# Kernel optimization log

Hardware: AMD Instinct MI355X
Metric: run time of the kernel (lower is better)

The kernel has to match this reference:

```python
import jax, jax.numpy as jnp
import numpy as np

N = 100000     # total points
PBS = 500      # point_batch_size (hard-coded in module)
K = 100        # num_neighbors
KP = 15        # num_kernel_points
EPS = 1e-5


def _bn(x, g, b, axes):
    # torch BatchNorm in training mode: batch stats, biased variance
    m = jnp.mean(x, axis=axes, keepdims=True)
    v = jnp.var(x, axis=axes, keepdims=True)
    return (x - m) / jnp.sqrt(v + EPS) * g + b


def setup_inputs() -> dict:
    key = jax.random.key(0)
    ks = jax.random.split(key, 16)
    rn = lambda k, sh, s=1.0: jax.random.normal(k, sh, jnp.float32) * s
    return {
        "pts": rn(ks[0], (N, 3)),
        "normal": rn(ks[1], (N, 3)),
        "kp_points": rn(ks[2], (KP, 3)),
        "kp_weights": rn(ks[3], (KP, 3, 128), 0.3),
        "kp_sigma": jnp.float32(1.0),
        "conv1_w": rn(ks[4], (1024, 128), 128 ** -0.5),
        "conv1_b": rn(ks[5], (1024,), 0.02),
        "bn1_g": jnp.ones((1024,), jnp.float32),
        "bn1_b": jnp.zeros((1024,), jnp.float32),
        "fc1_w": rn(ks[6], (512, 1024), 1024 ** -0.5),
        "fc1_b": rn(ks[7], (512,), 0.02),
        "bn4_g": jnp.ones((512,), jnp.float32),
        "bn4_b": jnp.zeros((512,), jnp.float32),
        "fc2_w": rn(ks[8], (256, 512), 512 ** -0.5),
        "fc2_b": rn(ks[9], (256,), 0.02),
        "bn5_g": jnp.ones((256,), jnp.float32),
        "bn5_b": jnp.zeros((256,), jnp.float32),
        "fc3_w": rn(ks[10], (3, 256), 256 ** -0.5),
        "fc3_b": rn(ks[11], (3,), 0.02),
        "index": jax.random.randint(ks[12], (PBS,), 0, N, jnp.int32),
    }


def reference(pts, normal, kp_points, kp_weights, kp_sigma,
              conv1_w, conv1_b, bn1_g, bn1_b,
              fc1_w, fc1_b, bn4_g, bn4_b,
              fc2_w, fc2_b, bn5_g, bn5_b,
              fc3_w, fc3_b, index):
    sel = pts[index]                                               # [B,3]
    # L-inf pairwise distance and kNN (topk of -dist, as in the torch code)
    dist = jnp.max(jnp.abs(sel[:, None, :] - pts[None, :, :]), axis=-1)  # [B,N]
    _, nbr = jax.lax.top_k(-dist, K)                               # [B,K]
    rel = pts[nbr] - sel[:, None, :]                               # [B,K,3]

    # KPConv: gaussian weights vs kernel points, per-kernel-point linear map
    d2 = jnp.sum((rel[:, :, None, :] - kp_points[None, None]) ** 2, axis=-1)  # [B,K,KP]
    w = jnp.exp(-0.5 * d2 / (kp_sigma ** 2))
    wf = rel[:, :, None, :] * w[..., None]                         # [B,K,KP,3]
    h = jax.nn.relu(jnp.einsum('bnkc,kco->bno', wf, kp_weights))   # [B,K,128]

    # 1x1 conv 128->1024, relu then BN over (batch, points) per channel
    h = jnp.einsum('bnc,oc->bno', h, conv1_w) + conv1_b            # [B,K,1024]
    h = _bn(jax.nn.relu(h), bn1_g, bn1_b, (0, 1))
    feat = jnp.max(h, axis=1)                                      # [B,1024]

    feat = _bn(jax.nn.relu(feat @ fc1_w.T + fc1_b), bn4_g, bn4_b, (0,))
    feat = _bn(jax.nn.relu(feat @ fc2_w.T + fc2_b), bn5_g, bn5_b, (0,))
    feat = feat @ fc3_w.T + fc3_b                                  # [B,3]
    return feat, normal[index]
```

## Files before the change

kernel.cpp:

```cpp
#include <hip/hip_runtime.h>
#include <hip/hip_fp16.h>

#define NPTS 100000
#define NB 500
#define KNN 100
#define KPN 15
#define C1 128
#define C2 1024
#define C3 512
#define C4 256

#define G 64
#define NCELLS (G * G * G)
#define GB 5.0f
#define GINVH ((float)G / (2.f * GB))
#define CAND_CAP 2048

typedef _Float16 half8 __attribute__((ext_vector_type(8)));
typedef float f32x4 __attribute__((ext_vector_type(4)));

__device__ __forceinline__ int cell_coord(float x) {
  int c = (int)floorf((x + GB) * GINVH);
  return min(max(c, 0), G - 1);
}
__device__ __forceinline__ int cell_of(float x, float y, float z) {
  return (cell_coord(x) << 12) | (cell_coord(y) << 6) | cell_coord(z);
}

__global__ __launch_bounds__(256) void prep_kernel(
    const float* __restrict__ pts, const float* __restrict__ normal,
    const int* __restrict__ index, const float* __restrict__ w1,
    const float* __restrict__ kpw, float* __restrict__ sel,
    float* __restrict__ out2, __half* __restrict__ wh,
    __half* __restrict__ kpwT_hi, __half* __restrict__ kpwT_lo,
    unsigned* __restrict__ cnt) {
  int i = blockIdx.x * 256 + threadIdx.x;
  if (i < NB) {
    int ix = index[i];
    sel[i * 3 + 0] = pts[3 * ix + 0];
    sel[i * 3 + 1] = pts[3 * ix + 1];
    sel[i * 3 + 2] = pts[3 * ix + 2];
    out2[i * 3 + 0] = normal[3 * ix + 0];
    out2[i * 3 + 1] = normal[3 * ix + 1];
    out2[i * 3 + 2] = normal[3 * ix + 2];
  }
  if (i < C2 * C1) wh[i] = __float2half(w1[i]);
  if (i < 128 * 64) {
    int o = i >> 6, j = i & 63;
    float v = (j < 45) ? kpw[j * 128 + o] : 0.f;
    __half hi = __float2half_rn(v);
    kpwT_hi[i] = hi;
    kpwT_lo[i] = __float2half_rn(v - __half2float(hi));
  }
  if (i < NPTS)
    atomicAdd(&cnt[cell_of(pts[3 * i], pts[3 * i + 1], pts[3 * i + 2])], 1u);
}

__global__ __launch_bounds__(256) void grid_scan1_kernel(
    const unsigned* __restrict__ cnt, unsigned* __restrict__ cursor,
    unsigned* __restrict__ chunktot) {
  const int tid = threadIdx.x;
  int base = blockIdx.x * 1024 + tid * 4;
  unsigned c0 = cnt[base], c1 = cnt[base + 1], c2 = cnt[base + 2],
           c3 = cnt[base + 3];
  unsigned tot = c0 + c1 + c2 + c3;
  __shared__ unsigned sb[256];
  sb[tid] = tot;
  __syncthreads();
  for (int off = 1; off < 256; off <<= 1) {
    unsigned add = (tid >= off) ? sb[tid - off] : 0u;
    __syncthreads();
    sb[tid] += add;
    __syncthreads();
  }
  unsigned excl = sb[tid] - tot;
  cursor[base] = excl;
  cursor[base + 1] = excl + c0;
  cursor[base + 2] = excl + c0 + c1;
  cursor[base + 3] = excl + c0 + c1 + c2;
  if (tid == 255) chunktot[blockIdx.x] = sb[255];
}

__global__ __launch_bounds__(256) void grid_scan2_kernel(
    const unsigned* __restrict__ chunktot, unsigned* __restrict__ chunkoff) {
  const int tid = threadIdx.x;
  unsigned v = chunktot[tid];
  __shared__ unsigned sb[256];
  sb[tid] = v;
  __syncthreads();
  for (int off = 1; off < 256; off <<= 1) {
    unsigned add = (tid >= off) ? sb[tid - off] : 0u;
    __syncthreads();
    sb[tid] += add;
    __syncthreads();
  }
  chunkoff[tid] = sb[tid] - v;
}

__global__ __launch_bounds__(256) void grid_scan3_kernel(
    unsigned* __restrict__ cursor, const unsigned* __restrict__ chunkoff) {
  unsigned off = chunkoff[blockIdx.x];
  int base = blockIdx.x * 1024 + threadIdx.x * 4;
#pragma unroll
  for (int j = 0; j < 4; ++j) cursor[base + j] += off;
}

__global__ __launch_bounds__(256) void grid_scatter_kernel(
    const float* __restrict__ pts, unsigned* __restrict__ cursor,
    float4* __restrict__ sorted) {
  int i = blockIdx.x * 256 + threadIdx.x;
  if (i >= NPTS) return;
  float x = pts[3 * i], y = pts[3 * i + 1], z = pts[3 * i + 2];
  unsigned pos = atomicAdd(&cursor[cell_of(x, y, z)], 1u);
  sorted[pos] = make_float4(x, y, z, __int_as_float(i));
}

__device__ __forceinline__ unsigned linf_bits(float px, float py, float pz,
                                              float sx, float sy, float sz) {
  float dx = fabsf(px - sx), dy = fabsf(py - sy), dz = fabsf(pz - sz);
  return __float_as_uint(fmaxf(fmaxf(dx, dy), dz));
}

__global__ __launch_bounds__(256) void knn_kernel(
    const float4* __restrict__ sorted, const unsigned* __restrict__ cnt,
    const unsigned* __restrict__ cursor,
    const float* __restrict__ sel, int* __restrict__ nbr) {
  const int b = blockIdx.x;
  const int tid = threadIdx.x;
  __shared__ unsigned cbits[CAND_CAP];
  __shared__ int cidx[CAND_CAP];
  __shared__ unsigned hist[4096];
  __shared__ unsigned scanbuf[256];
  __shared__ int s_total, s_m, s_mc, s_chunk;
  __shared__ unsigned s_excl, s_bub;

  const float qx = sel[b * 3 + 0], qy = sel[b * 3 + 1], qz = sel[b * 3 + 2];
  const int qcx = cell_coord(qx), qcy = cell_coord(qy), qcz = cell_coord(qz);

  if (tid == 0) s_total = 0;
  __syncthreads();
  int s = 1;
  int pxlo = 1, pxhi = 0, pylo = 1, pyhi = 0, pzlo = 1, pzhi = 0;
  int xlo, xhi, ylo, yhi, zlo, zhi;
  for (;;) {
    xlo = max(qcx - s, 0); xhi = min(qcx + s, G - 1);
    ylo = max(qcy - s, 0); yhi = min(qcy + s, G - 1);
    zlo = max(qcz - s, 0); zhi = min(qcz + s, G - 1);
    int nx = xhi - xlo + 1, ny = yhi - ylo + 1, nz = zhi - zlo + 1;
    int ncell = nx * ny * nz;
    unsigned local = 0;
    for (int ci = tid; ci < ncell; ci += 256) {
      int cz = ci % nz;
      int r = ci / nz;
      int cy = r % ny;
      int cx = r / ny;
      int ax = xlo + cx, ay = ylo + cy, az = zlo + cz;
      if (ax >= pxlo && ax <= pxhi && ay >= pylo && ay <= pyhi &&
          az >= pzlo && az <= pzhi)
        continue;
      local += cnt[(ax << 12) | (ay << 6) | az];
    }
#pragma unroll
    for (int off = 32; off; off >>= 1) local += __shfl_down(local, off);
    if ((tid & 63) == 0) atomicAdd(&s_total, (int)local);
    __syncthreads();
    if (s_total >= KNN || (xlo == 0 && ylo == 0 && zlo == 0 && xhi == G - 1 &&
                           yhi == G - 1 && zhi == G - 1))
      break;
    pxlo = xlo; pxhi = xhi; pylo = ylo; pyhi = yhi; pzlo = zlo; pzhi = zhi;
    ++s;
    __syncthreads();
  }

  if (tid == 0) s_m = 0;
  __syncthreads();
  {
    int nx = xhi - xlo + 1, ny = yhi - ylo + 1, nz = zhi - zlo + 1;
    int ncell = nx * ny * nz;
    for (int ci = tid; ci < ncell; ci += 256) {
      int cz = ci % nz;
      int r = ci / nz;
      int cy = r % ny;
      int cx = r / ny;
      int cell = ((xlo + cx) << 12) | ((ylo + cy) << 6) | (zlo + cz);
      unsigned end = cursor[cell];
      unsigned beg = end - cnt[cell];
      int k = (int)(end - beg);
      if (k > 0) {
        int e0 = atomicAdd(&s_m, k);
        for (unsigned p = beg; p < end; ++p, ++e0) {
          if (e0 < CAND_CAP) {
            float4 f = sorted[p];
            cbits[e0] = linf_bits(f.x, f.y, f.z, qx, qy, qz);
            cidx[e0] = __float_as_int(f.w);
          }
        }
      }
    }
  }
  __syncthreads();
  int m = s_m < CAND_CAP ? s_m : CAND_CAP;

  for (int j = tid; j < 4096; j += 256) hist[j] = 0;
  __syncthreads();
  for (int e = tid; e < m; e += 256) atomicAdd(&hist[cbits[e] >> 19], 1u);
  __syncthreads();
  unsigned csum = 0;
  {
    int c0 = tid * 16;
#pragma unroll
    for (int j = 0; j < 16; ++j) csum += hist[c0 + j];
  }
  scanbuf[tid] = csum;
  __syncthreads();
  for (int off = 1; off < 256; off <<= 1) {
    unsigned add = (tid >= off) ? scanbuf[tid - off] : 0u;
    __syncthreads();
    scanbuf[tid] += add;
    __syncthreads();
  }
  {
    unsigned incl = scanbuf[tid], excl = incl - csum;
    if (excl < KNN && KNN <= incl) {
      s_chunk = tid;
      s_excl = excl;
    }
  }
  __syncthreads();
  if (tid == 0) {
    unsigned cum = s_excl;
    int bin = s_chunk * 16;
    while (cum + hist[bin] < KNN) {
      cum += hist[bin];
      ++bin;
    }
    s_bub = (unsigned)(bin + 1) << 19;
  }
  __syncthreads();

  const unsigned bub = s_bub;
  const float dub = __uint_as_float(bub);
  if (tid == 0) s_mc = 0;
  __syncthreads();
  {
    int xlo2 = min(max((int)floorf((qx - dub + GB) * GINVH), 0), G - 1);
    int xhi2 = min(max((int)floorf((qx + dub + GB) * GINVH), 0), G - 1);
    int ylo2 = min(max((int)floorf((qy - dub + GB) * GINVH), 0), G - 1);
    int yhi2 = min(max((int)floorf((qy + dub + GB) * GINVH), 0), G - 1);
    int zlo2 = min(max((int)floorf((qz - dub + GB) * GINVH), 0), G - 1);
    int zhi2 = min(max((int)floorf((qz + dub + GB) * GINVH), 0), G - 1);
    int nx = xhi2 - xlo2 + 1, ny = yhi2 - ylo2 + 1, nz = zhi2 - zlo2 + 1;
    int ncell = nx * ny * nz;
    for (int ci = tid; ci < ncell; ci += 256) {
      int cz = ci % nz;
      int r = ci / nz;
      int cy = r % ny;
      int cx = r / ny;
      int cell = ((xlo2 + cx) << 12) | ((ylo2 + cy) << 6) | (zlo2 + cz);
      unsigned end = cursor[cell];
      unsigned beg = end - cnt[cell];
      for (unsigned p = beg; p < end; ++p) {
        float4 f = sorted[p];
        unsigned bits = linf_bits(f.x, f.y, f.z, qx, qy, qz);
        if (bits < bub) {
          int e = atomicAdd(&s_mc, 1);
          if (e < CAND_CAP) {
            cbits[e] = bits;
            cidx[e] = __float_as_int(f.w);
          }
        }
      }
    }
  }
  __syncthreads();
  int mc = s_mc < CAND_CAP ? s_mc : CAND_CAP;

  for (int c = tid; c < mc; c += 256) {
    unsigned bc = cbits[c];
    int ic = cidx[c];
    int rank = 0;
    for (int j = 0; j < mc; ++j) {
      unsigned bj = cbits[j];
      rank += (bj < bc || (bj == bc && cidx[j] < ic)) ? 1 : 0;
    }
    if (rank < KNN) nbr[b * KNN + rank] = ic;
  }
}

__global__ __launch_bounds__(512) void kpconv_conv1_kernel(
    const float* __restrict__ pts, const float* __restrict__ sel,
    const int* __restrict__ nbr, const float* __restrict__ kp_points,
    const __half* __restrict__ kpwT_hi, const __half* __restrict__ kpwT_lo,
    const float* __restrict__ kp_sigma, const __half* __restrict__ wh,
    const float* __restrict__ bias, float* __restrict__ featmax,
    float* __restrict__ featmin, float* __restrict__ bnsum,
    float* __restrict__ bnsq) {
  const int b = blockIdx.x;
  const int tid = threadIdx.x;
  const int wave = tid >> 6, lane = tid & 63;
  const int lr = lane & 15, quad = lane >> 4;

  __shared__ __align__(16) char smem[71168];
  __half* As_hi = (__half*)smem;
  __half* As_lo = As_hi + 112 * 72;
  __half* Bs_hi = As_lo + 112 * 72;
  __half* Bs_lo = Bs_hi + 128 * 72;
  float* rel = (float*)(Bs_lo + 128 * 72);
  float* kpp = rel + 100 * 4;
  __half* Hs = (__half*)smem;
  __half* Ws = Hs + 112 * 136;

  for (int i = tid; i < 128 * 8; i += 512) {
    int row = i >> 3, seg = i & 7;
    *(float4*)&Bs_hi[row * 72 + seg * 8] =
        *(const float4*)&kpwT_hi[row * 64 + seg * 8];
    *(float4*)&Bs_lo[row * 72 + seg * 8] =
        *(const float4*)&kpwT_lo[row * 64 + seg * 8];
  }
  {
    float4 z = make_float4(0.f, 0.f, 0.f, 0.f);
    for (int i = tid; i < 112 * 8; i += 512) {
      int row = i >> 3, seg = i & 7;
      *(float4*)&As_hi[row * 72 + seg * 8] = z;
      *(float4*)&As_lo[row * 72 + seg * 8] = z;
    }
  }
  if (tid < 45) kpp[tid] = kp_points[tid];
  if (tid < 100) {
    int idx = nbr[b * KNN + tid];
    rel[tid * 4 + 0] = pts[3 * idx + 0] - sel[b * 3 + 0];
    rel[tid * 4 + 1] = pts[3 * idx + 1] - sel[b * 3 + 1];
    rel[tid * 4 + 2] = pts[3 * idx + 2] - sel[b * 3 + 2];
  }
  __syncthreads();

  const float sg = kp_sigma[0];
  const float inv2s2 = -0.5f / (sg * sg);
  for (int i = tid; i < 100 * KPN; i += 512) {
    int k = i / KPN, p = i - k * KPN;
    float rx = rel[k * 4 + 0] - kpp[p * 3 + 0];
    float ry = rel[k * 4 + 1] - kpp[p * 3 + 1];
    float rz = rel[k * 4 + 2] - kpp[p * 3 + 2];
    float w = expf(inv2s2 * (rx * rx + ry * ry + rz * rz));
#pragma unroll
    for (int c = 0; c < 3; ++c) {
      float a = rel[k * 4 + c] * w;
      __half hi = __float2half_rn(a);
      As_hi[k * 72 + p * 3 + c] = hi;
      As_lo[k * 72 + p * 3 + c] = __float2half_rn(a - __half2float(hi));
    }
  }
  __syncthreads();

  f32x4 acc1[7];
#pragma unroll
  for (int m = 0; m < 7; ++m) acc1[m] = (f32x4)(0.f);
#pragma unroll
  for (int s = 0; s < 2; ++s) {
    int boff = (wave * 16 + lr) * 72 + s * 32 + quad * 8;
    half8 bhi = *(const half8*)&Bs_hi[boff];
    half8 blo = *(const half8*)&Bs_lo[boff];
#pragma unroll
    for (int m = 0; m < 7; ++m) {
      int aoff = (m * 16 + lr) * 72 + s * 32 + quad * 8;
      half8 ahi = *(const half8*)&As_hi[aoff];
      half8 alo = *(const half8*)&As_lo[aoff];
      acc1[m] = __builtin_amdgcn_mfma_f32_16x16x32_f16(ahi, bhi, acc1[m], 0, 0, 0);
      acc1[m] = __builtin_amdgcn_mfma_f32_16x16x32_f16(ahi, blo, acc1[m], 0, 0, 0);
      acc1[m] = __builtin_amdgcn_mfma_f32_16x16x32_f16(alo, bhi, acc1[m], 0, 0, 0);
    }
  }
  __syncthreads();

  {
    int col = wave * 16 + lr;
#pragma unroll
    for (int m = 0; m < 7; ++m)
#pragma unroll
      for (int r = 0; r < 4; ++r) {
        int row = m * 16 + quad * 4 + r;
        Hs[row * 136 + col] = __float2half_rn(fmaxf(acc1[m][r], 0.f));
      }
  }

  for (int c = 0; c < 8; ++c) {
    __syncthreads();
    for (int i = tid; i < 128 * 16; i += 512) {
      int row = i >> 4, seg = i & 15;
      *(float4*)&Ws[row * 136 + seg * 8] =
          *(const float4*)&wh[(c * 128 + row) * 128 + seg * 8];
    }
    __syncthreads();

    f32x4 acc2[7];
#pragma unroll
    for (int m = 0; m < 7; ++m) acc2[m] = (f32x4)(0.f);
#pragma unroll
    for (int s = 0; s < 4; ++s) {
      half8 bfrag =
          *(const half8*)&Ws[(wave * 16 + lr) * 136 + s * 32 + quad * 8];
#pragma unroll
      for (int m = 0; m < 7; ++m) {
        half8 afrag =
            *(const half8*)&Hs[(m * 16 + lr) * 136 + s * 32 + quad * 8];
        acc2[m] = __builtin_amdgcn_mfma_f32_16x16x32_f16(afrag, bfrag,
                                                         acc2[m], 0, 0, 0);
      }
    }

    {
      int col = c * 128 + wave * 16 + lr;
      float bv = bias[col];
      float pmax = -1e30f, pmin = 1e30f, psum = 0.f, psq = 0.f;
#pragma unroll
      for (int m = 0; m < 7; ++m)
#pragma unroll
        for (int r = 0; r < 4; ++r) {
          int row = m * 16 + quad * 4 + r;
          if (row < 100) {
            float y = fmaxf(acc2[m][r] + bv, 0.f);
            pmax = fmaxf(pmax, y);
            pmin = fminf(pmin, y);
            psum += y;
            psq += y * y;
          }
        }
      pmax = fmaxf(pmax, __shfl_xor(pmax, 16));
      pmax = fmaxf(pmax, __shfl_xor(pmax, 32));
      pmin = fminf(pmin, __shfl_xor(pmin, 16));
      pmin = fminf(pmin, __shfl_xor(pmin, 32));
      psum += __shfl_xor(psum, 16);
      psum += __shfl_xor(psum, 32);
      psq += __shfl_xor(psq, 16);
      psq += __shfl_xor(psq, 32);
      if (quad == 0) {
        featmax[b * C2 + col] = pmax;
        featmin[b * C2 + col] = pmin;
        atomicAdd(&bnsum[col], psum);
        atomicAdd(&bnsq[col], psq);
      }
    }
  }
}

__global__ __launch_bounds__(256) void fc1_kernel(
    const float* __restrict__ featmax, const float* __restrict__ featmin,
    const float* __restrict__ bnsum, const float* __restrict__ bnsq,
    const float* __restrict__ g, const float* __restrict__ bb,
    const float* __restrict__ w,
    const float* __restrict__ bias, float* __restrict__ yraw,
    float* __restrict__ s, float* __restrict__ sq) {
  const int r0 = blockIdx.x * 4;
  const int n0 = blockIdx.y * 64;
  const int tid = threadIdx.x;
  const int col = tid >> 2;
  const int row = tid & 3;
  __shared__ float xs[4][1028];
  __shared__ float ws[64][132];
  __shared__ float amul[C2], badd[C2];
  const float invn = 1.f / (float)(NB * KNN);
  for (int o = tid; o < C2; o += 256) {
    float m = bnsum[o] * invn;
    float v = bnsq[o] * invn - m * m;
    float a = g[o] / sqrtf(v + 1e-5f);
    amul[o] = a;
    badd[o] = bb[o] - m * a;
  }
  __syncthreads();
  for (int f = tid; f < C2; f += 256) {
    int rr = f >> 8, kq = (f & 255) * 4;
    float4 mx = *(const float4*)&featmax[(r0 + rr) * C2 + kq];
    float4 mn = *(const float4*)&featmin[(r0 + rr) * C2 + kq];
    float4 o4;
    o4.x = (amul[kq + 0] >= 0.f ? mx.x : mn.x) * amul[kq + 0] + badd[kq + 0];
    o4.y = (amul[kq + 1] >= 0.f ? mx.y : mn.y) * amul[kq + 1] + badd[kq + 1];
    o4.z = (amul[kq + 2] >= 0.f ? mx.z : mn.z) * amul[kq + 2] + badd[kq + 2];
    o4.w = (amul[kq + 3] >= 0.f ? mx.w : mn.w) * amul[kq + 3] + badd[kq + 3];
    *(float4*)&xs[rr][kq] = o4;
  }
  float acc = 0.f;
  for (int kc = 0; kc < C2; kc += 128) {
    __syncthreads();
#pragma unroll
    for (int i = 0; i < 8; ++i) {
      int f = tid + i * 256;
      int cr = f >> 5, kq = (f & 31) * 4;
      *(float4*)&ws[cr][kq] = *(const float4*)&w[(n0 + cr) * C2 + kc + kq];
    }
    __syncthreads();
    for (int kk = 0; kk < 128; kk += 4) {
      float4 xv = *(float4*)&xs[row][kc + kk];
      float4 wv = *(float4*)&ws[col][kk];
      acc += xv.x * wv.x + xv.y * wv.y + xv.z * wv.z + xv.w * wv.w;
    }
  }
  float y = fmaxf(acc + bias[n0 + col], 0.f);
  yraw[(r0 + row) * C3 + n0 + col] = y;
  float ys = y, y2 = y * y;
  ys += __shfl_xor(ys, 1); y2 += __shfl_xor(y2, 1);
  ys += __shfl_xor(ys, 2); y2 += __shfl_xor(y2, 2);
  if (row == 0) {
    atomicAdd(&s[n0 + col], ys);
    atomicAdd(&sq[n0 + col], y2);
  }
}

__global__ __launch_bounds__(256) void fc2_kernel(
    const float* __restrict__ x,
    const float* __restrict__ bnsum, const float* __restrict__ bnsq,
    const float* __restrict__ g, const float* __restrict__ bb,
    const float* __restrict__ w,
    const float* __restrict__ bias, float* __restrict__ yraw,
    float* __restrict__ s, float* __restrict__ sq) {
  const int r0 = blockIdx.x * 4;
  const int n0 = blockIdx.y * 64;
  const int tid = threadIdx.x;
  const int col = tid >> 2;
  const int row = tid & 3;
  __shared__ float xs[4][516];
  __shared__ float ws[64][132];
  __shared__ float amul[C3], badd[C3];
  const float invn = 1.f / (float)NB;
  for (int o = tid; o < C3; o += 256) {
    float m = bnsum[o] * invn;
    float v = bnsq[o] * invn - m * m;
    float a = g[o] / sqrtf(v + 1e-5f);
    amul[o] = a;
    badd[o] = bb[o] - m * a;
  }
  __syncthreads();
  for (int f = tid; f < C3; f += 256) {
    int rr = f >> 7, kq = (f & 127) * 4;
    float4 xv = *(const float4*)&x[(r0 + rr) * C3 + kq];
    float4 o4;
    o4.x = xv.x * amul[kq + 0] + badd[kq + 0];
    o4.y = xv.y * amul[kq + 1] + badd[kq + 1];
    o4.z = xv.z * amul[kq + 2] + badd[kq + 2];
    o4.w = xv.w * amul[kq + 3] + badd[kq + 3];
    *(float4*)&xs[rr][kq] = o4;
  }
  float acc = 0.f;
  for (int kc = 0; kc < C3; kc += 128) {
    __syncthreads();
#pragma unroll
    for (int i = 0; i < 8; ++i) {
      int f = tid + i * 256;
      int cr = f >> 5, kq = (f & 31) * 4;
      *(float4*)&ws[cr][kq] = *(const float4*)&w[(n0 + cr) * C3 + kc + kq];
    }
    __syncthreads();
    for (int kk = 0; kk < 128; kk += 4) {
      float4 xv = *(float4*)&xs[row][kc + kk];
      float4 wv = *(float4*)&ws[col][kk];
      acc += xv.x * wv.x + xv.y * wv.y + xv.z * wv.z + xv.w * wv.w;
    }
  }
  float y = fmaxf(acc + bias[n0 + col], 0.f);
  yraw[(r0 + row) * C4 + n0 + col] = y;
  float ys = y, y2 = y * y;
  ys += __shfl_xor(ys, 1); y2 += __shfl_xor(y2, 1);
  ys += __shfl_xor(ys, 2); y2 += __shfl_xor(y2, 2);
  if (row == 0) {
    atomicAdd(&s[n0 + col], ys);
    atomicAdd(&sq[n0 + col], y2);
  }
}

__global__ __launch_bounds__(256) void fc3_kernel(
    const float* __restrict__ x,
    const float* __restrict__ bnsum, const float* __restrict__ bnsq,
    const float* __restrict__ g, const float* __restrict__ bb,
    const float* __restrict__ w, const float* __restrict__ bias,
    float* __restrict__ out) {
  const int tid = threadIdx.x;
  __shared__ float pmul[C4], padd[C4];
  {
    const float invn = 1.f / (float)NB;
    float m = bnsum[tid] * invn;
    float v = bnsq[tid] * invn - m * m;
    float a = g[tid] / sqrtf(v + 1e-5f);
    pmul[tid] = a;
    padd[tid] = bb[tid] - m * a;
  }
  __syncthreads();
  int idx = blockIdx.x * 256 + tid;
  if (idx >= NB * 3) return;
  int b = idx / 3, o = idx % 3;
  float acc = 0.f;
  for (int k = 0; k < C4; ++k)
    acc += (x[b * C4 + k] * pmul[k] + padd[k]) * w[o * C4 + k];
  out[idx] = acc + bias[o];
}

extern "C" void kernel_launch(void* const* d_in, const int* in_sizes, int n_in,
                              void* d_out, int out_size, void* d_ws,
                              size_t ws_size, hipStream_t stream) {
  const float* pts = (const float*)d_in[0];
  const float* normal = (const float*)d_in[1];
  const float* kp_points = (const float*)d_in[2];
  const float* kp_weights = (const float*)d_in[3];
  const float* kp_sigma = (const float*)d_in[4];
  const float* conv1_w = (const float*)d_in[5];
  const float* conv1_b = (const float*)d_in[6];
  const float* bn1_g = (const float*)d_in[7];
  const float* bn1_b = (const float*)d_in[8];
  const float* fc1_w = (const float*)d_in[9];
  const float* fc1_b = (const float*)d_in[10];
  const float* bn4_g = (const float*)d_in[11];
  const float* bn4_b = (const float*)d_in[12];
  const float* fc2_w = (const float*)d_in[13];
  const float* fc2_b = (const float*)d_in[14];
  const float* bn5_g = (const float*)d_in[15];
  const float* bn5_b = (const float*)d_in[16];
  const float* fc3_w = (const float*)d_in[17];
  const float* fc3_b = (const float*)d_in[18];
  const int* index = (const int*)d_in[19];
  float* out = (float*)d_out;

  char* p = (char*)d_ws;
  auto carve = [&](size_t bytes) {
    void* r = (void*)p;
    p += (bytes + 255) & ~(size_t)255;
    return r;
  };
  float* sel = (float*)carve(NB * 3 * 4);
  int* nbr = (int*)carve(NB * KNN * 4);
  __half* wh = (__half*)carve((size_t)C2 * C1 * 2);
  __half* kpwT_hi = (__half*)carve((size_t)128 * 64 * 2);
  __half* kpwT_lo = (__half*)carve((size_t)128 * 64 * 2);
  float* featmax = (float*)carve(NB * C2 * 4);
  float* featmin = (float*)carve(NB * C2 * 4);
  float* f2raw = (float*)carve(NB * C3 * 4);
  float* f3raw = (float*)carve(NB * C4 * 4);
  float* stats = (float*)carve((2 * C2 + 2 * C3 + 2 * C4) * 4);
  float* bnsum = stats;
  float* bnsq = stats + C2;
  float* s4 = stats + 2 * C2;
  float* sq4 = s4 + C3;
  float* s5 = sq4 + C3;
  float* sq5 = s5 + C4;
  unsigned* cellcnt = (unsigned*)carve((size_t)NCELLS * 4);
  unsigned* cellcur = (unsigned*)carve((size_t)NCELLS * 4);
  unsigned* chunktot = (unsigned*)carve(256 * 4);
  unsigned* chunkoff = (unsigned*)carve(256 * 4);
  float4* sortedpts = (float4*)carve((size_t)NPTS * 16);

  hipMemsetAsync(stats, 0, (2 * C2 + 2 * C3 + 2 * C4) * 4, stream);
  hipMemsetAsync(cellcnt, 0, (size_t)NCELLS * 4, stream);

  prep_kernel<<<(C2 * C1 + 255) / 256, 256, 0, stream>>>(
      pts, normal, index, conv1_w, kp_weights, sel, out + NB * 3, wh, kpwT_hi,
      kpwT_lo, cellcnt);
  grid_scan1_kernel<<<256, 256, 0, stream>>>(cellcnt, cellcur, chunktot);
  grid_scan2_kernel<<<1, 256, 0, stream>>>(chunktot, chunkoff);
  grid_scan3_kernel<<<256, 256, 0, stream>>>(cellcur, chunkoff);
  grid_scatter_kernel<<<(NPTS + 255) / 256, 256, 0, stream>>>(pts, cellcur,
                                                              sortedpts);
  knn_kernel<<<NB, 256, 0, stream>>>(sortedpts, cellcnt, cellcur, sel, nbr);
  kpconv_conv1_kernel<<<NB, 512, 0, stream>>>(
      pts, sel, nbr, kp_points, kpwT_hi, kpwT_lo, kp_sigma, wh, conv1_b,
      featmax, featmin, bnsum, bnsq);
  fc1_kernel<<<dim3(125, C3 / 64), 256, 0, stream>>>(
      featmax, featmin, bnsum, bnsq, bn1_g, bn1_b, fc1_w, fc1_b, f2raw, s4,
      sq4);
  fc2_kernel<<<dim3(125, C4 / 64), 256, 0, stream>>>(
      f2raw, s4, sq4, bn4_g, bn4_b, fc2_w, fc2_b, f3raw, s5, sq5);
  fc3_kernel<<<(NB * 3 + 255) / 256, 256, 0, stream>>>(
      f3raw, s5, sq5, bn5_g, bn5_b, fc3_w, fc3_b, out);
}
```

Measured before the change: 303.1 us.

## Move fc1 to split-fp16 MFMA with separate BN1-normalize kernel

Replaces the scalar FP32 fc1 GEMM with an MFMA kernel that emulates fp32 by splitting inputs and weights into hi/lo fp16 parts and issuing three MFMAs per step. A new elementwise kernel applies BN1 and writes the hi/lo halves of the activations, and the prep kernel now also splits fc1 weights, which enlarges its grid. This cuts ALU time for the 500x1024x512 GEMM but adds an extra launch and extra global traffic. The grid is only 64 blocks, which limits parallelism.

```diff
diff --git a/kernel.cpp b/kernel.cpp
--- a/kernel.cpp
+++ b/kernel.cpp
@@ -30,10 +30,11 @@
 __global__ __launch_bounds__(256) void prep_kernel(
     const float* __restrict__ pts, const float* __restrict__ normal,
     const int* __restrict__ index, const float* __restrict__ w1,
-    const float* __restrict__ kpw, float* __restrict__ sel,
-    float* __restrict__ out2, __half* __restrict__ wh,
-    __half* __restrict__ kpwT_hi, __half* __restrict__ kpwT_lo,
-    unsigned* __restrict__ cnt) {
+    const float* __restrict__ kpw, const float* __restrict__ fc1w,
+    float* __restrict__ sel, float* __restrict__ out2,
+    __half* __restrict__ wh, __half* __restrict__ kpwT_hi,
+    __half* __restrict__ kpwT_lo, __half* __restrict__ fwhi,
+    __half* __restrict__ fwlo, unsigned* __restrict__ cnt) {
   int i = blockIdx.x * 256 + threadIdx.x;
   if (i < NB) {
     int ix = index[i];
@@ -51,6 +52,12 @@
     __half hi = __float2half_rn(v);
     kpwT_hi[i] = hi;
     kpwT_lo[i] = __float2half_rn(v - __half2float(hi));
+  }
+  if (i < C3 * C2) {
+    float v = fc1w[i];
+    __half hi = __float2half_rn(v);
+    fwhi[i] = hi;
+    fwlo[i] = __float2half_rn(v - __half2float(hi));
   }
   if (i < NPTS)
     atomicAdd(&cnt[cell_of(pts[3 * i], pts[3 * i + 1], pts[3 * i + 2])], 1u);
@@ -443,65 +450,102 @@
   }
 }
 
-__global__ __launch_bounds__(256) void fc1_kernel(
+__global__ __launch_bounds__(256) void bn1half_kernel(
     const float* __restrict__ featmax, const float* __restrict__ featmin,
     const float* __restrict__ bnsum, const float* __restrict__ bnsq,
     const float* __restrict__ g, const float* __restrict__ bb,
-    const float* __restrict__ w,
+    __half* __restrict__ Xhi, __half* __restrict__ Xlo) {
+  int idx = blockIdx.x * 256 + threadIdx.x;
+  if (idx >= NB * C2) return;
+  int o = idx & (C2 - 1);
+  const float invn = 1.f / (float)(NB * KNN);
+  float m = bnsum[o] * invn;
+  float v = bnsq[o] * invn - m * m;
+  float a = g[o] / sqrtf(v + 1e-5f);
+  float x = (a >= 0.f) ? featmax[idx] : featmin[idx];
+  float y = (x - m) * a + bb[o];
+  __half hi = __float2half_rn(y);
+  Xhi[idx] = hi;
+  Xlo[idx] = __float2half_rn(y - __half2float(hi));
+}
+
+__global__ __launch_bounds__(256) void fc1_mfma_kernel(
+    const __half* __restrict__ Xhi, const __half* __restrict__ Xlo,
+    const __half* __restrict__ Whi, const __half* __restrict__ Wlo,
     const float* __restrict__ bias, float* __restrict__ yraw,
     float* __restrict__ s, float* __restrict__ sq) {
-  const int r0 = blockIdx.x * 4;
+  const int r0 = blockIdx.x * 64;
   const int n0 = blockIdx.y * 64;
   const int tid = threadIdx.x;
-  const int col = tid >> 2;
-  const int row = tid & 3;
-  __shared__ float xs[4][1028];
-  __shared__ float ws[64][132];
-  __shared__ float amul[C2], badd[C2];
-  const float invn = 1.f / (float)(NB * KNN);
-  for (int o = tid; o < C2; o += 256) {
-    float m = bnsum[o] * invn;
-    float v = bnsq[o] * invn - m * m;
-    float a = g[o] / sqrtf(v + 1e-5f);
-    amul[o] = a;
-    badd[o] = bb[o] - m * a;
-  }
-  __syncthreads();
-  for (int f = tid; f < C2; f += 256) {
-    int rr = f >> 8, kq = (f & 255) * 4;
-    float4 mx = *(const float4*)&featmax[(r0 + rr) * C2 + kq];
-    float4 mn = *(const float4*)&featmin[(r0 + rr) * C2 + kq];
-    float4 o4;
-    o4.x = (amul[kq + 0] >= 0.f ? mx.x : mn.x) * amul[kq + 0] + badd[kq + 0];
-    o4.y = (amul[kq + 1] >= 0.f ? mx.y : mn.y) * amul[kq + 1] + badd[kq + 1];
-    o4.z = (amul[kq + 2] >= 0.f ? mx.z : mn.z) * amul[kq + 2] + badd[kq + 2];
-    o4.w = (amul[kq + 3] >= 0.f ? mx.w : mn.w) * amul[kq + 3] + badd[kq + 3];
-    *(float4*)&xs[rr][kq] = o4;
-  }
-  float acc = 0.f;
-  for (int kc = 0; kc < C2; kc += 128) {
-    __syncthreads();
-#pragma unroll
-    for (int i = 0; i < 8; ++i) {
-      int f = tid + i * 256;
-      int cr = f >> 5, kq = (f & 31) * 4;
-      *(float4*)&ws[cr][kq] = *(const float4*)&w[(n0 + cr) * C2 + kc + kq];
-    }
-    __syncthreads();
-    for (int kk = 0; kk < 128; kk += 4) {
-      float4 xv = *(float4*)&xs[row][kc + kk];
-      float4 wv = *(float4*)&ws[col][kk];
-      acc += xv.x * wv.x + xv.y * wv.y + xv.z * wv.z + xv.w * wv.w;
-    }
-  }
-  float y = fmaxf(acc + bias[n0 + col], 0.f);
-  yraw[(r0 + row) * C3 + n0 + col] = y;
-  float ys = y, y2 = y * y;
-  ys += __shfl_xor(ys, 1); y2 += __shfl_xor(y2, 1);
-  ys += __shfl_xor(ys, 2); y2 += __shfl_xor(y2, 2);
-  if (row == 0) {
-    atomicAdd(&s[n0 + col], ys);
-    atomicAdd(&sq[n0 + col], y2);
+  const int wave = tid >> 6, lane = tid & 63;
+  const int lr = lane & 15, quad = lane >> 4;
+  __shared__ __half Xs_hi[64 * 72], Xs_lo[64 * 72];
+  __shared__ __half Ws_hi[64 * 72], Ws_lo[64 * 72];
+
+  f32x4 acc[4];
+#pragma unroll
+  for (int m = 0; m < 4; ++m) acc[m] = (f32x4)(0.f);
+
+  for (int kc = 0; kc < C2; kc += 64) {
+    __syncthreads();
+    for (int i = tid; i < 64 * 8; i += 256) {
+      int row = i >> 3, seg = i & 7;
+      int gr = r0 + row;
+      float4 vhi = make_float4(0.f, 0.f, 0.f, 0.f), vlo = vhi;
+      if (gr < NB) {
+        vhi = *(const float4*)&Xhi[gr * C2 + kc + seg * 8];
+        vlo = *(const float4*)&Xlo[gr * C2 + kc + seg * 8];
+      }
+      *(float4*)&Xs_hi[row * 72 + seg * 8] = vhi;
+      *(float4*)&Xs_lo[row * 72 + seg * 8] = vlo;
+      *(float4*)&Ws_hi[row * 72 + seg * 8] =
+          *(const float4*)&Whi[(n0 + row) * C2 + kc + seg * 8];
+      *(float4*)&Ws_lo[row * 72 + seg * 8] =
+          *(const float4*)&Wlo[(n0 + row) * C2 + kc + seg * 8];
+    }
+    __syncthreads();
+
+#pragma unroll
+    for (int s2 = 0; s2 < 2; ++s2) {
+      int boff = (wave * 16 + lr) * 72 + s2 * 32 + quad * 8;
+      half8 bhi = *(const half8*)&Ws_hi[boff];
+      half8 blo = *(const half8*)&Ws_lo[boff];
+#pragma unroll
+      for (int m = 0; m < 4; ++m) {
+        int aoff = (m * 16 + lr) * 72 + s2 * 32 + quad * 8;
+        half8 ahi = *(const half8*)&Xs_hi[aoff];
+        half8 alo = *(const half8*)&Xs_lo[aoff];
+        acc[m] = __builtin_amdgcn_mfma_f32_16x16x32_f16(ahi, bhi, acc[m], 0, 0, 0);
+        acc[m] = __builtin_amdgcn_mfma_f32_16x16x32_f16(ahi, blo, acc[m], 0, 0, 0);
+        acc[m] = __builtin_amdgcn_mfma_f32_16x16x32_f16(alo, bhi, acc[m], 0, 0, 0);
+      }
+    }
+  }
+
+  {
+    int col = n0 + wave * 16 + lr;
+    float bv = bias[col];
+    float psum = 0.f, psq = 0.f;
+#pragma unroll
+    for (int m = 0; m < 4; ++m)
+#pragma unroll
+      for (int r = 0; r < 4; ++r) {
+        int row = r0 + m * 16 + quad * 4 + r;
+        if (row < NB) {
+          float y = fmaxf(acc[m][r] + bv, 0.f);
+          yraw[row * C3 + col] = y;
+          psum += y;
+          psq += y * y;
+        }
+      }
+    psum += __shfl_xor(psum, 16);
+    psum += __shfl_xor(psum, 32);
+    psq += __shfl_xor(psq, 16);
+    psq += __shfl_xor(psq, 32);
+    if (quad == 0) {
+      atomicAdd(&s[col], psum);
+      atomicAdd(&sq[col], psq);
+    }
   }
 }
 
@@ -628,6 +672,10 @@
   __half* wh = (__half*)carve((size_t)C2 * C1 * 2);
   __half* kpwT_hi = (__half*)carve((size_t)128 * 64 * 2);
   __half* kpwT_lo = (__half*)carve((size_t)128 * 64 * 2);
+  __half* fwhi = (__half*)carve((size_t)C3 * C2 * 2);
+  __half* fwlo = (__half*)carve((size_t)C3 * C2 * 2);
+  __half* Xhi = (__half*)carve((size_t)NB * C2 * 2);
+  __half* Xlo = (__half*)carve((size_t)NB * C2 * 2);
   float* featmax = (float*)carve(NB * C2 * 4);
   float* featmin = (float*)carve(NB * C2 * 4);
   float* f2raw = (float*)carve(NB * C3 * 4);
@@ -648,9 +696,9 @@
   hipMemsetAsync(stats, 0, (2 * C2 + 2 * C3 + 2 * C4) * 4, stream);
   hipMemsetAsync(cellcnt, 0, (size_t)NCELLS * 4, stream);
 
-  prep_kernel<<<(C2 * C1 + 255) / 256, 256, 0, stream>>>(
-      pts, normal, index, conv1_w, kp_weights, sel, out + NB * 3, wh, kpwT_hi,
-      kpwT_lo, cellcnt);
+  prep_kernel<<<(C3 * C2 + 255) / 256, 256, 0, stream>>>(
+      pts, normal, index, conv1_w, kp_weights, fc1_w, sel, out + NB * 3, wh,
+      kpwT_hi, kpwT_lo, fwhi, fwlo, cellcnt);
   grid_scan1_kernel<<<256, 256, 0, stream>>>(cellcnt, cellcur, chunktot);
   grid_scan2_kernel<<<1, 256, 0, stream>>>(chunktot, chunkoff);
   grid_scan3_kernel<<<256, 256, 0, stream>>>(cellcur, chunkoff);
@@ -660,9 +708,10 @@
   kpconv_conv1_kernel<<<NB, 512, 0, stream>>>(
       pts, sel, nbr, kp_points, kpwT_hi, kpwT_lo, kp_sigma, wh, conv1_b,
       featmax, featmin, bnsum, bnsq);
-  fc1_kernel<<<dim3(125, C3 / 64), 256, 0, stream>>>(
-      featmax, featmin, bnsum, bnsq, bn1_g, bn1_b, fc1_w, fc1_b, f2raw, s4,
-      sq4);
+  bn1half_kernel<<<(NB * C2 + 255) / 256, 256, 0, stream>>>(
+      featmax, featmin, bnsum, bnsq, bn1_g, bn1_b, Xhi, Xlo);
+  fc1_mfma_kernel<<<dim3(8, 8), 256, 0, stream>>>(Xhi, Xlo, fwhi, fwlo, fc1_b,
+                                                  f2raw, s4, sq4);
   fc2_kernel<<<dim3(125, C4 / 64), 256, 0, stream>>>(
       f2raw, s4, sq4, bn4_g, bn4_b, fc2_w, fc2_b, f3raw, s5, sq5);
   fc3_kernel<<<(NB * 3 + 255) / 256, 256, 0, stream>>>(
```

Result: faster. 266.2 us (-12.2%).
